# Kernel optimization log

Measured on AMD Instinct MI355X. Metric: run time of the kernel, lower is better.

The kernel has to match this reference:

```python
import jax, jax.numpy as jnp
import numpy as np

N, D, E, C = 100000, 256, 262144, 5


def setup_inputs() -> dict:
    key = jax.random.key(0)
    ks = jax.random.split(key, 8)
    s = 1.0 / np.sqrt(D)
    return {
        "node_feat": jax.random.normal(ks[0], (N, D), jnp.float32),
        "pair_idx": jax.random.randint(ks[1], (E, 2), 0, N, dtype=jnp.int64)
        if jax.config.jax_enable_x64 else jax.random.randint(ks[1], (E, 2), 0, N, dtype=jnp.int32),
        "W_agg": jax.random.normal(ks[2], (2 * D, D), jnp.float32) * (1.0 / np.sqrt(2 * D)),
        "b_agg": jnp.zeros((D,), jnp.float32),
        "We1": jax.random.normal(ks[3], (D, D), jnp.float32) * s,
        "be1": jnp.zeros((D,), jnp.float32),
        "We2": jax.random.normal(ks[4], (D, C), jnp.float32) * s,
        "be2": jnp.zeros((C,), jnp.float32),
        "Wn1": jax.random.normal(ks[5], (D, D), jnp.float32) * s,
        "bn1": jnp.zeros((D,), jnp.float32),
        "Wn2": jax.random.normal(ks[6], (D, 2), jnp.float32) * s,
        "bn2": jnp.zeros((2,), jnp.float32),
    }


def reference(node_feat, pair_idx, W_agg, b_agg, We1, be1, We2, be2, Wn1, bn1, Wn2, bn2):
    # node_predictor: Linear -> ReLU -> Linear (D -> D -> 2)
    node_res = jnp.maximum(node_feat @ Wn1 + bn1, 0.0) @ Wn2 + bn2  # [N, 2]

    # gather node-pair features for both directed orderings (x,y) and (y,x)
    src = node_feat[pair_idx[:, 0]]  # [E, D]
    dst = node_feat[pair_idx[:, 1]]  # [E, D]
    # edge_feat_agger(cat(src,dst)) + edge_feat_agger(cat(dst,src))
    ef_fwd = jnp.concatenate([src, dst], axis=-1) @ W_agg + b_agg  # [E, D]
    ef_bwd = jnp.concatenate([dst, src], axis=-1) @ W_agg + b_agg  # [E, D]
    ed_feat = ef_fwd + ef_bwd

    # edge_predictor: Linear -> ReLU -> Linear (D -> D -> C)
    pred_edge = jnp.maximum(ed_feat @ We1 + be1, 0.0) @ We2 + be2  # [E, C]
    return node_res, pred_edge
```

## Files before the change

kernel.cpp:

```cpp
#include <hip/hip_runtime.h>

#define D 256

typedef float f32x4 __attribute__((ext_vector_type(4)));
typedef short short8 __attribute__((ext_vector_type(8)));
typedef __bf16 bf16x8 __attribute__((ext_vector_type(8)));

static __device__ __forceinline__ short f2bs(float f) {
    __bf16 b = (__bf16)f;
    return __builtin_bit_cast(short, b);
}
static __device__ __forceinline__ float bs2f(short s) {
    unsigned u = ((unsigned)(unsigned short)s) << 16;
    return __builtin_bit_cast(float, u);
}


__global__ void pre_bc(const float* __restrict__ b_agg, const float* __restrict__ We1,
                       const float* __restrict__ be1, float* __restrict__ bc)
{
    int j = threadIdx.x;
    float acc = be1[j];
    for (int k = 0; k < D; ++k)
        acc += 2.f * b_agg[k] * We1[k * D + j];
    bc[j] = acc;
}

__global__ void pre_wct(const float* __restrict__ W_agg, const float* __restrict__ We1,
                        short* __restrict__ WcT)
{
    __shared__ float wsrow[D];
    int i = blockIdx.x, j = threadIdx.x;
    wsrow[j] = W_agg[i * D + j] + W_agg[(i + D) * D + j];
    __syncthreads();
    float acc = 0.f;
    for (int k = 0; k < D; ++k)
        acc += wsrow[k] * We1[k * D + j];
    WcT[j * D + i] = f2bs(acc);
}

__global__ void pre_wn1t(const float* __restrict__ Wn1, short* __restrict__ Wn1T)
{
    int i = blockIdx.x, j = threadIdx.x;
    Wn1T[j * D + i] = f2bs(Wn1[i * D + j]);
}

__global__ void pre_w2t(const float* __restrict__ We2, const float* __restrict__ Wn2,
                        short* __restrict__ We2T, short* __restrict__ Wn2T)
{
    int k = threadIdx.x;
    for (int c = 0; c < 16; ++c) {
        float ve = (c < 5) ? We2[k * 5 + c] : 0.f;
        float vn = (c < 2) ? Wn2[k * 2 + c] : 0.f;
        We2T[c * D + k] = f2bs(ve);
        Wn2T[c * D + k] = f2bs(vn);
    }
}

__global__ __launch_bounds__(512, 2)
void node_h_gemm2(const float* __restrict__ nf,
                  const short* __restrict__ WcT, const short* __restrict__ Wn1T,
                  const float* __restrict__ bc,  const float* __restrict__ bn1,
                  const short* __restrict__ Wn2T, const float* __restrict__ bn2,
                  short* __restrict__ H, float* __restrict__ outn, int nrows)
{
    __shared__ __align__(16) short sA[2048 * 8];
    __shared__ __align__(16) short hl[64 * D];

    const int tid = threadIdx.x;
    const int lane = tid & 63;
    const int w = tid >> 6;
    const int l15 = lane & 15;
    const int g = lane >> 4;
    const int rowblk = blockIdx.x * 64;

    const short* Wb = (w < 4) ? WcT : Wn1T;
    const int nc0 = (w & 3) * 4;
    short8 Bw[4][8];
#pragma unroll
    for (int t = 0; t < 4; ++t)
#pragma unroll
        for (int ks = 0; ks < 8; ++ks)
            Bw[t][ks] = *reinterpret_cast<const short8*>(
                Wb + ((nc0 + t) * 16 + l15) * D + ks * 32 + g * 8);

#pragma unroll
    for (int j = 0; j < 4; ++j) {
        const int i = j * 512 + tid;
        const int li = i & 15, gi = (i >> 4) & 3, fi = (i >> 6) & 3, ki = i >> 8;
        int r = rowblk + fi * 16 + li;
        if (r > nrows - 1) r = nrows - 1;
        const float4* p = reinterpret_cast<const float4*>(nf + (size_t)r * D + ki * 32 + gi * 8);
        float4 x0 = p[0], x1 = p[1];
        bf16x8 v = {(__bf16)x0.x, (__bf16)x0.y, (__bf16)x0.z, (__bf16)x0.w,
                    (__bf16)x1.x, (__bf16)x1.y, (__bf16)x1.z, (__bf16)x1.w};
        *reinterpret_cast<short8*>(&sA[i * 8]) = __builtin_bit_cast(short8, v);
    }
    __syncthreads();

    f32x4 acc[4][4];
#pragma unroll
    for (int f = 0; f < 4; ++f)
#pragma unroll
        for (int t = 0; t < 4; ++t)
            acc[f][t] = f32x4{0.f, 0.f, 0.f, 0.f};

#pragma unroll
    for (int ks = 0; ks < 8; ++ks) {
        short8 a[4];
#pragma unroll
        for (int f = 0; f < 4; ++f)
            a[f] = *reinterpret_cast<const short8*>(&sA[(ks * 256 + f * 64 + lane) * 8]);
#pragma unroll
        for (int t = 0; t < 4; ++t)
#pragma unroll
            for (int f = 0; f < 4; ++f)
                acc[f][t] = __builtin_amdgcn_mfma_f32_16x16x32_bf16(a[f], Bw[t][ks], acc[f][t], 0, 0, 0);
    }

    if (w < 4) {
#pragma unroll
        for (int t = 0; t < 4; ++t) {
            const int col = w * 64 + t * 16 + l15;
            const float bb = 0.5f * bc[col];
#pragma unroll
            for (int f = 0; f < 4; ++f)
#pragma unroll
                for (int r = 0; r < 4; ++r) {
                    const int grow = rowblk + f * 16 + g * 4 + r;
                    if (grow < nrows)
                        H[(size_t)grow * D + col] = f2bs(acc[f][t][r] + bb);
                }
        }
    } else {
#pragma unroll
        for (int t = 0; t < 4; ++t) {
            const int col = (w - 4) * 64 + t * 16 + l15;
            const float bb = bn1[col];
            const int chunk = col >> 3;
#pragma unroll
            for (int f = 0; f < 4; ++f)
#pragma unroll
                for (int r = 0; r < 4; ++r) {
                    const int row = f * 16 + g * 4 + r;
                    float v = fmaxf(acc[f][t][r] + bb, 0.f);
                    hl[row * D + (((chunk ^ (row & 7)) << 3) | (col & 7))] = f2bs(v);
                }
        }
    }

    __syncthreads();

    if (w >= 4) {
        const int vr = w - 4;
        const int row = vr * 16 + l15;
        f32x4 a2 = f32x4{0.f, 0.f, 0.f, 0.f};
#pragma unroll
        for (int ks = 0; ks < 8; ++ks) {
            const int k0 = ks * 32 + g * 8;
            const int c = ks * 4 + g;
            short8 bw = *reinterpret_cast<const short8*>(Wn2T + l15 * D + k0);
            short8 ah = *reinterpret_cast<const short8*>(&hl[row * D + ((c ^ (row & 7)) * 8)]);
            a2 = __builtin_amdgcn_mfma_f32_16x16x32_bf16(ah, bw, a2, 0, 0, 0);
        }
        if (l15 < 2) {
            const float b2 = bn2[l15];
#pragma unroll
            for (int r = 0; r < 4; ++r) {
                const int grow = rowblk + vr * 16 + g * 4 + r;
                if (grow < nrows)
                    outn[(size_t)grow * 2 + l15] = a2[r] + b2;
            }
        }
    }
}

__global__ __launch_bounds__(256, 4)
void edge_gemv(const short* __restrict__ H, const int* __restrict__ pair,
               const short* __restrict__ We2T, const float* __restrict__ be2,
               float* __restrict__ out, int nedges)
{
    const int lane = threadIdx.x & 63;
    const int w = threadIdx.x >> 6;
    const int l15 = lane & 15;
    const int g = lane >> 4;

    short8 Bf[8];
#pragma unroll
    for (int ks = 0; ks < 8; ++ks)
        Bf[ks] = *reinterpret_cast<const short8*>(We2T + l15 * D + ks * 32 + g * 8);

    const float b2 = (l15 < 5) ? be2[l15] : 0.f;
    const int base = blockIdx.x * 256 + w * 64;

#pragma unroll
    for (int grp = 0; grp < 4; ++grp) {
        int e = base + grp * 16 + l15;
        if (e > nedges - 1) e = nedges - 1;
        const size_t si = (size_t)(unsigned)pair[2 * e];
        const size_t di = (size_t)(unsigned)pair[2 * e + 1];
        const short8* sp = reinterpret_cast<const short8*>(H + si * D + g * 8);
        const short8* dp = reinterpret_cast<const short8*>(H + di * D + g * 8);
        short8 sv[8], dv[8];
#pragma unroll
        for (int ks = 0; ks < 8; ++ks) {
            sv[ks] = sp[ks * 4];
            dv[ks] = dp[ks * 4];
        }
        f32x4 acc = f32x4{0.f, 0.f, 0.f, 0.f};
#pragma unroll
        for (int ks = 0; ks < 8; ++ks) {
            short8 a;
#pragma unroll
            for (int i = 0; i < 8; ++i)
                a[i] = f2bs(fmaxf(bs2f(sv[ks][i]) + bs2f(dv[ks][i]), 0.f));
            acc = __builtin_amdgcn_mfma_f32_16x16x32_bf16(a, Bf[ks], acc, 0, 0, 0);
        }
        if (l15 < 5) {
#pragma unroll
            for (int r = 0; r < 4; ++r) {
                const int ge = base + grp * 16 + g * 4 + r;
                if (ge < nedges)
                    out[(size_t)ge * 5 + l15] = acc[r] + b2;
            }
        }
    }
}

template<int MODE>
__global__ __launch_bounds__(256, 2)
void fused_mlp(const float* __restrict__ feat,
               const int* __restrict__ pair,
               const short* __restrict__ W1T,
               const float* __restrict__ bias1,
               const short* __restrict__ W2T,
               const float* __restrict__ bias2,
               float* __restrict__ out,
               int nrows, int ncols)
{
    __shared__ short hl[128 * D];

    const int tid = threadIdx.x;
    const int lane = tid & 63;
    const int w = tid >> 6;
    const int l15 = lane & 15;
    const int g = lane >> 4;
    const int rowblk = blockIdx.x * 128 + w * 32;

    const float* ap0[2];
    const float* ap1[2];
#pragma unroll
    for (int f = 0; f < 2; ++f) {
        int r = rowblk + f * 16 + l15;
        if (r > nrows - 1) r = nrows - 1;
        if constexpr (MODE == 0) {
            ap0[f] = feat + (size_t)r * D;
            ap1[f] = nullptr;
        } else {
            ap0[f] = feat + (size_t)pair[2 * r] * D;
            ap1[f] = feat + (size_t)pair[2 * r + 1] * D;
        }
    }

    f32x4 acc[2][16];
#pragma unroll
    for (int f = 0; f < 2; ++f)
#pragma unroll
        for (int t = 0; t < 16; ++t)
            acc[f][t] = f32x4{0.f, 0.f, 0.f, 0.f};

#pragma unroll
    for (int ks = 0; ks < 8; ++ks) {
        const int k0 = ks * 32 + g * 8;
        short8 af[2];
#pragma unroll
        for (int f = 0; f < 2; ++f) {
            const float4* p0 = reinterpret_cast<const float4*>(ap0[f] + k0);
            float4 x0 = p0[0], x1 = p0[1];
            if constexpr (MODE == 1) {
                const float4* p1 = reinterpret_cast<const float4*>(ap1[f] + k0);
                float4 y0 = p1[0], y1 = p1[1];
                x0.x += y0.x; x0.y += y0.y; x0.z += y0.z; x0.w += y0.w;
                x1.x += y1.x; x1.y += y1.y; x1.z += y1.z; x1.w += y1.w;
            }
            bf16x8 bv = {(__bf16)x0.x, (__bf16)x0.y, (__bf16)x0.z, (__bf16)x0.w,
                         (__bf16)x1.x, (__bf16)x1.y, (__bf16)x1.z, (__bf16)x1.w};
            af[f] = __builtin_bit_cast(short8, bv);
        }
#pragma unroll
        for (int t = 0; t < 16; ++t) {
            short8 bw = *reinterpret_cast<const short8*>(W1T + ((t * 16 + l15) * D + k0));
            acc[0][t] = __builtin_amdgcn_mfma_f32_16x16x32_bf16(af[0], bw, acc[0][t], 0, 0, 0);
            acc[1][t] = __builtin_amdgcn_mfma_f32_16x16x32_bf16(af[1], bw, acc[1][t], 0, 0, 0);
        }
    }

#pragma unroll
    for (int t = 0; t < 16; ++t) {
        const int col = t * 16 + l15;
        const float b = bias1[col];
        const int chunk = col >> 3;
#pragma unroll
        for (int f = 0; f < 2; ++f) {
#pragma unroll
            for (int r = 0; r < 4; ++r) {
                const int rl = w * 32 + f * 16 + g * 4 + r;
                float v = fmaxf(acc[f][t][r] + b, 0.f);
                hl[rl * D + ((chunk ^ (rl & 7)) << 3) + (col & 7)] = f2bs(v);
            }
        }
    }

    __syncthreads();

    f32x4 acc2[2];
    acc2[0] = f32x4{0.f, 0.f, 0.f, 0.f};
    acc2[1] = f32x4{0.f, 0.f, 0.f, 0.f};
#pragma unroll
    for (int ks = 0; ks < 8; ++ks) {
        const int k0 = ks * 32 + g * 8;
        const int chunk = k0 >> 3;
        short8 bw = *reinterpret_cast<const short8*>(W2T + (l15 * D + k0));
#pragma unroll
        for (int f = 0; f < 2; ++f) {
            const int rl = w * 32 + f * 16 + l15;
            short8 ah = *reinterpret_cast<const short8*>(&hl[rl * D + ((chunk ^ (rl & 7)) << 3)]);
            acc2[f] = __builtin_amdgcn_mfma_f32_16x16x32_bf16(ah, bw, acc2[f], 0, 0, 0);
        }
    }

    if (l15 < ncols) {
        const float b2 = bias2[l15];
#pragma unroll
        for (int f = 0; f < 2; ++f) {
#pragma unroll
            for (int r = 0; r < 4; ++r) {
                const int grow = rowblk + f * 16 + g * 4 + r;
                if (grow < nrows)
                    out[(size_t)grow * ncols + l15] = acc2[f][r] + b2;
            }
        }
    }
}


extern "C" void kernel_launch(void* const* d_in, const int* in_sizes, int n_in,
                              void* d_out, int out_size, void* d_ws, size_t ws_size,
                              hipStream_t stream)
{
    const float* node_feat = (const float*)d_in[0];
    const int*   pair_idx  = (const int*)d_in[1];
    const float* W_agg     = (const float*)d_in[2];
    const float* b_agg     = (const float*)d_in[3];
    const float* We1       = (const float*)d_in[4];
    const float* be1       = (const float*)d_in[5];
    const float* We2       = (const float*)d_in[6];
    const float* be2       = (const float*)d_in[7];
    const float* Wn1       = (const float*)d_in[8];
    const float* bn1       = (const float*)d_in[9];
    const float* Wn2       = (const float*)d_in[10];
    const float* bn2       = (const float*)d_in[11];

    const int N = in_sizes[0] / D;
    const int E = in_sizes[1] / 2;

    float* out = (float*)d_out;
    char*  ws  = (char*)d_ws;

    short* WcT  = (short*)(ws + 0);
    short* Wn1T = (short*)(ws + 131072);
    short* We2T = (short*)(ws + 262144);
    short* Wn2T = (short*)(ws + 270336);
    float* bc   = (float*)(ws + 278528);
    const size_t H_OFF = 524288;
    short* H = (short*)(ws + H_OFF);
    const size_t need = H_OFF + (size_t)N * D * 2;

    pre_bc<<<1, 256, 0, stream>>>(b_agg, We1, be1, bc);
    pre_wct<<<D, 256, 0, stream>>>(W_agg, We1, WcT);
    pre_wn1t<<<D, 256, 0, stream>>>(Wn1, Wn1T);
    pre_w2t<<<1, 256, 0, stream>>>(We2, Wn2, We2T, Wn2T);

    if (ws_size >= need) {
        node_h_gemm2<<<(N + 63) / 64, 512, 0, stream>>>(
            node_feat, WcT, Wn1T, bc, bn1, Wn2T, bn2, H, out, N);

        edge_gemv<<<(E + 255) / 256, 256, 0, stream>>>(
            H, pair_idx, We2T, be2, out + (size_t)2 * N, E);
    } else {
        fused_mlp<0><<<(N + 127) / 128, 256, 0, stream>>>(
            node_feat, nullptr, Wn1T, bn1, Wn2T, bn2, out, N, 2);

        fused_mlp<1><<<E / 128, 256, 0, stream>>>(
            node_feat, pair_idx, WcT, bc, We2T, be2, out + (size_t)2 * N, E, 5);
    }
}
```

Before: 168.4 us.

## Stream weights through LDS with async loads and stage edge gathers in LDS

The node GEMM now uses 1024-thread blocks. Each warp holds a 32-column slice instead of keeping a full weight slice in registers, and the weights stream through double-buffered LDS with global_load_lds. H is staged in LDS and written out as coalesced 16-byte rows. The edge kernel gathers src/dst H rows straight into XOR-swizzled LDS with async loads, using shuffled indices, before the MFMA. This lowers register pressure and makes the gathers coalesced, at the cost of more LDS traffic and per-k-step barriers. The code relies on WcT and Wn1T being contiguous in the workspace, so it can index 32 column groups from a single WT pointer.

Measured after the change: 186.7 us. 1.11x slower.

```diff
diff --git a/kernel.cpp b/kernel.cpp
--- a/kernel.cpp
+++ b/kernel.cpp
@@ -13,6 +13,13 @@
 static __device__ __forceinline__ float bs2f(short s) {
     unsigned u = ((unsigned)(unsigned short)s) << 16;
     return __builtin_bit_cast(float, u);
+}
+
+static __device__ __forceinline__ void gload_lds16(const short* g, short* l) {
+    __builtin_amdgcn_global_load_lds(
+        (const __attribute__((address_space(1))) void*)g,
+        (__attribute__((address_space(3))) void*)l,
+        16, 0, 0);
 }
 
 
@@ -57,15 +64,15 @@
     }
 }
 
-__global__ __launch_bounds__(512, 2)
-void node_h_gemm2(const float* __restrict__ nf,
-                  const short* __restrict__ WcT, const short* __restrict__ Wn1T,
+__global__ __launch_bounds__(1024)
+void node_h_gemm3(const float* __restrict__ nf,
+                  const short* __restrict__ WT,
                   const float* __restrict__ bc,  const float* __restrict__ bn1,
                   const short* __restrict__ Wn2T, const float* __restrict__ bn2,
                   short* __restrict__ H, float* __restrict__ outn, int nrows)
 {
     __shared__ __align__(16) short sA[2048 * 8];
-    __shared__ __align__(16) short hl[64 * D];
+    __shared__ __align__(16) short sB[2][2048 * 8];
 
     const int tid = threadIdx.x;
     const int lane = tid & 63;
@@ -74,19 +81,9 @@
     const int g = lane >> 4;
     const int rowblk = blockIdx.x * 64;
 
-    const short* Wb = (w < 4) ? WcT : Wn1T;
-    const int nc0 = (w & 3) * 4;
-    short8 Bw[4][8];
-#pragma unroll
-    for (int t = 0; t < 4; ++t)
-#pragma unroll
-        for (int ks = 0; ks < 8; ++ks)
-            Bw[t][ks] = *reinterpret_cast<const short8*>(
-                Wb + ((nc0 + t) * 16 + l15) * D + ks * 32 + g * 8);
-
-#pragma unroll
-    for (int j = 0; j < 4; ++j) {
-        const int i = j * 512 + tid;
+#pragma unroll
+    for (int j = 0; j < 2; ++j) {
+        const int i = j * 1024 + tid;
         const int li = i & 15, gi = (i >> 4) & 3, fi = (i >> 6) & 3, ki = i >> 8;
         int r = rowblk + fi * 16 + li;
         if (r > nrows - 1) r = nrows - 1;
@@ -96,46 +93,74 @@
                     (__bf16)x1.x, (__bf16)x1.y, (__bf16)x1.z, (__bf16)x1.w};
         *reinterpret_cast<short8*>(&sA[i * 8]) = __builtin_bit_cast(short8, v);
     }
+#pragma unroll
+    for (int j = 0; j < 2; ++j) {
+        const int v = j * 1024 + tid;
+        const int nc = v >> 6, vl = v & 15, vg = (v >> 4) & 3;
+        gload_lds16(WT + (nc * 16 + vl) * D + vg * 8,
+                    &sB[0][(j * 1024 + w * 64) * 8]);
+    }
+    asm volatile("s_waitcnt vmcnt(0)" ::: "memory");
     __syncthreads();
 
-    f32x4 acc[4][4];
+    f32x4 acc[4][2];
 #pragma unroll
     for (int f = 0; f < 4; ++f)
 #pragma unroll
-        for (int t = 0; t < 4; ++t)
+        for (int t = 0; t < 2; ++t)
             acc[f][t] = f32x4{0.f, 0.f, 0.f, 0.f};
 
+    int cur = 0;
 #pragma unroll
     for (int ks = 0; ks < 8; ++ks) {
-        short8 a[4];
+        if (ks < 7) {
+#pragma unroll
+            for (int j = 0; j < 2; ++j) {
+                const int v = j * 1024 + tid;
+                const int nc = v >> 6, vl = v & 15, vg = (v >> 4) & 3;
+                gload_lds16(WT + (nc * 16 + vl) * D + (ks + 1) * 32 + vg * 8,
+                            &sB[cur ^ 1][(j * 1024 + w * 64) * 8]);
+            }
+        }
+        short8 a[4], b[2];
 #pragma unroll
         for (int f = 0; f < 4; ++f)
             a[f] = *reinterpret_cast<const short8*>(&sA[(ks * 256 + f * 64 + lane) * 8]);
 #pragma unroll
-        for (int t = 0; t < 4; ++t)
+        for (int t = 0; t < 2; ++t)
+            b[t] = *reinterpret_cast<const short8*>(&sB[cur][((w * 2 + t) * 64 + lane) * 8]);
+#pragma unroll
+        for (int t = 0; t < 2; ++t)
 #pragma unroll
             for (int f = 0; f < 4; ++f)
-                acc[f][t] = __builtin_amdgcn_mfma_f32_16x16x32_bf16(a[f], Bw[t][ks], acc[f][t], 0, 0, 0);
-    }
-
-    if (w < 4) {
-#pragma unroll
-        for (int t = 0; t < 4; ++t) {
-            const int col = w * 64 + t * 16 + l15;
+                acc[f][t] = __builtin_amdgcn_mfma_f32_16x16x32_bf16(a[f], b[t], acc[f][t], 0, 0, 0);
+        if (ks < 7) {
+            asm volatile("s_waitcnt vmcnt(0)" ::: "memory");
+            __syncthreads();
+            cur ^= 1;
+        }
+    }
+
+    __syncthreads();
+
+    short* sH = (short*)sB;
+    if (w < 8) {
+#pragma unroll
+        for (int t = 0; t < 2; ++t) {
+            const int col = w * 32 + t * 16 + l15;
             const float bb = 0.5f * bc[col];
 #pragma unroll
             for (int f = 0; f < 4; ++f)
 #pragma unroll
                 for (int r = 0; r < 4; ++r) {
-                    const int grow = rowblk + f * 16 + g * 4 + r;
-                    if (grow < nrows)
-                        H[(size_t)grow * D + col] = f2bs(acc[f][t][r] + bb);
+                    const int row = f * 16 + g * 4 + r;
+                    sH[row * D + col] = f2bs(acc[f][t][r] + bb);
                 }
         }
     } else {
 #pragma unroll
-        for (int t = 0; t < 4; ++t) {
-            const int col = (w - 4) * 64 + t * 16 + l15;
+        for (int t = 0; t < 2; ++t) {
+            const int col = (w - 8) * 32 + t * 16 + l15;
             const float bb = bn1[col];
             const int chunk = col >> 3;
 #pragma unroll
@@ -144,15 +169,24 @@
                 for (int r = 0; r < 4; ++r) {
                     const int row = f * 16 + g * 4 + r;
                     float v = fmaxf(acc[f][t][r] + bb, 0.f);
-                    hl[row * D + (((chunk ^ (row & 7)) << 3) | (col & 7))] = f2bs(v);
+                    sA[row * D + (((chunk ^ (row & 7)) << 3) | (col & 7))] = f2bs(v);
                 }
         }
     }
 
     __syncthreads();
 
-    if (w >= 4) {
-        const int vr = w - 4;
+#pragma unroll
+    for (int j = 0; j < 2; ++j) {
+        const int u = j * 1024 + tid;
+        const int row = u >> 5, seg = u & 31;
+        if (rowblk + row < nrows)
+            *reinterpret_cast<short8*>(H + (size_t)(rowblk + row) * D + seg * 8) =
+                *reinterpret_cast<const short8*>(&sH[u * 8]);
+    }
+
+    if (w >= 8 && w < 12) {
+        const int vr = w - 8;
         const int row = vr * 16 + l15;
         f32x4 a2 = f32x4{0.f, 0.f, 0.f, 0.f};
 #pragma unroll
@@ -160,7 +194,7 @@
             const int k0 = ks * 32 + g * 8;
             const int c = ks * 4 + g;
             short8 bw = *reinterpret_cast<const short8*>(Wn2T + l15 * D + k0);
-            short8 ah = *reinterpret_cast<const short8*>(&hl[row * D + ((c ^ (row & 7)) * 8)]);
+            short8 ah = *reinterpret_cast<const short8*>(&sA[row * D + ((c ^ (row & 7)) * 8)]);
             a2 = __builtin_amdgcn_mfma_f32_16x16x32_bf16(ah, bw, a2, 0, 0, 0);
         }
         if (l15 < 2) {
@@ -175,54 +209,61 @@
     }
 }
 
-__global__ __launch_bounds__(256, 4)
-void edge_gemv(const short* __restrict__ H, const int* __restrict__ pair,
-               const short* __restrict__ We2T, const float* __restrict__ be2,
-               float* __restrict__ out, int nedges)
-{
+__global__ __launch_bounds__(256)
+void edge_gemv2(const short* __restrict__ H, const int* __restrict__ pair,
+                const short* __restrict__ We2T, const float* __restrict__ be2,
+                float* __restrict__ out, int nedges)
+{
+    __shared__ __align__(16) short eb[4][32 * D];
+
     const int lane = threadIdx.x & 63;
     const int w = threadIdx.x >> 6;
     const int l15 = lane & 15;
     const int g = lane >> 4;
+    const int base = blockIdx.x * 64 + w * 16;
 
     short8 Bf[8];
 #pragma unroll
     for (int ks = 0; ks < 8; ++ks)
         Bf[ks] = *reinterpret_cast<const short8*>(We2T + l15 * D + ks * 32 + g * 8);
 
-    const float b2 = (l15 < 5) ? be2[l15] : 0.f;
-    const int base = blockIdx.x * 256 + w * 64;
-
-#pragma unroll
-    for (int grp = 0; grp < 4; ++grp) {
-        int e = base + grp * 16 + l15;
-        if (e > nedges - 1) e = nedges - 1;
-        const size_t si = (size_t)(unsigned)pair[2 * e];
-        const size_t di = (size_t)(unsigned)pair[2 * e + 1];
-        const short8* sp = reinterpret_cast<const short8*>(H + si * D + g * 8);
-        const short8* dp = reinterpret_cast<const short8*>(H + di * D + g * 8);
-        short8 sv[8], dv[8];
-#pragma unroll
-        for (int ks = 0; ks < 8; ++ks) {
-            sv[ks] = sp[ks * 4];
-            dv[ks] = dp[ks * 4];
-        }
-        f32x4 acc = f32x4{0.f, 0.f, 0.f, 0.f};
-#pragma unroll
-        for (int ks = 0; ks < 8; ++ks) {
-            short8 a;
-#pragma unroll
-            for (int i = 0; i < 8; ++i)
-                a[i] = f2bs(fmaxf(bs2f(sv[ks][i]) + bs2f(dv[ks][i]), 0.f));
-            acc = __builtin_amdgcn_mfma_f32_16x16x32_bf16(a, Bf[ks], acc, 0, 0, 0);
-        }
-        if (l15 < 5) {
-#pragma unroll
-            for (int r = 0; r < 4; ++r) {
-                const int ge = base + grp * 16 + g * 4 + r;
-                if (ge < nedges)
-                    out[(size_t)ge * 5 + l15] = acc[r] + b2;
-            }
+    int pv = 0;
+    {
+        int pi = 2 * base + lane;
+        const int pmax = 2 * nedges - 1;
+        if (lane < 32) pv = pair[pi > pmax ? pmax : pi];
+    }
+
+    const int rsub = lane >> 5;
+    const int pos = lane & 31;
+#pragma unroll
+    for (int j = 0; j < 16; ++j) {
+        const int ridx = __shfl(pv, 2 * j + rsub);
+        const int c = pos ^ (j & 7);
+        gload_lds16(H + (size_t)(unsigned)ridx * D + c * 8, &eb[w][(2 * j) * D]);
+    }
+    asm volatile("s_waitcnt vmcnt(0)" ::: "memory");
+
+    f32x4 acc = f32x4{0.f, 0.f, 0.f, 0.f};
+#pragma unroll
+    for (int ks = 0; ks < 8; ++ks) {
+        const int slot = (ks * 4 + g) ^ (l15 & 7);
+        short8 sv = *reinterpret_cast<const short8*>(&eb[w][(2 * l15) * D + slot * 8]);
+        short8 dv = *reinterpret_cast<const short8*>(&eb[w][(2 * l15 + 1) * D + slot * 8]);
+        short8 a;
+#pragma unroll
+        for (int i = 0; i < 8; ++i)
+            a[i] = f2bs(fmaxf(bs2f(sv[i]) + bs2f(dv[i]), 0.f));
+        acc = __builtin_amdgcn_mfma_f32_16x16x32_bf16(a, Bf[ks], acc, 0, 0, 0);
+    }
+
+    if (l15 < 5) {
+        const float b2 = be2[l15];
+#pragma unroll
+        for (int r = 0; r < 4; ++r) {
+            const int ge = base + g * 4 + r;
+            if (ge < nedges)
+                out[(size_t)ge * 5 + l15] = acc[r] + b2;
         }
     }
 }
@@ -382,10 +423,10 @@
     pre_w2t<<<1, 256, 0, stream>>>(We2, Wn2, We2T, Wn2T);
 
     if (ws_size >= need) {
-        node_h_gemm2<<<(N + 63) / 64, 512, 0, stream>>>(
-            node_feat, WcT, Wn1T, bc, bn1, Wn2T, bn2, H, out, N);
-
-        edge_gemv<<<(E + 255) / 256, 256, 0, stream>>>(
+        node_h_gemm3<<<(N + 63) / 64, 1024, 0, stream>>>(
+            node_feat, WcT, bc, bn1, Wn2T, bn2, H, out, N);
+
+        edge_gemv2<<<(E + 63) / 64, 256, 0, stream>>>(
             H, pair_idx, We2T, be2, out + (size_t)2 * N, E);
     } else {
         fused_mlp<0><<<(N + 127) / 128, 256, 0, stream>>>(
```

## Stage H stores via LDS and gather edge rows with global_load_lds

Applied to the files above, without the earlier changes.

The node GEMM now writes its H tile into shared memory first and then stores it to global memory as coalesced 16-byte rows, replacing scattered 2-byte stores. The edge kernel gathers source and destination H rows with direct global-to-LDS loads into a swizzled buffer, 16 edges per wave, and then reads MFMA operands from LDS. This aims to improve gather coalescing and memory-level parallelism. The cost is more LDS per block (64KB for the edge kernel), which limits occupancy, plus an extra barrier in the node kernel.

After: 187.1 us. 1.11x slower.

```diff
diff --git a/kernel.cpp b/kernel.cpp
--- a/kernel.cpp
+++ b/kernel.cpp
@@ -13,6 +13,13 @@
 static __device__ __forceinline__ float bs2f(short s) {
     unsigned u = ((unsigned)(unsigned short)s) << 16;
     return __builtin_bit_cast(float, u);
+}
+
+static __device__ __forceinline__ void gload_lds16(const short* g, short* l) {
+    __builtin_amdgcn_global_load_lds(
+        (const __attribute__((address_space(1))) void*)g,
+        (__attribute__((address_space(3))) void*)l,
+        16, 0, 0);
 }
 
 
@@ -58,7 +65,7 @@
 }
 
 __global__ __launch_bounds__(512, 2)
-void node_h_gemm2(const float* __restrict__ nf,
+void node_h_gemm4(const float* __restrict__ nf,
                   const short* __restrict__ WcT, const short* __restrict__ Wn1T,
                   const float* __restrict__ bc,  const float* __restrict__ bn1,
                   const short* __restrict__ Wn2T, const float* __restrict__ bn2,
@@ -83,6 +90,11 @@
         for (int ks = 0; ks < 8; ++ks)
             Bw[t][ks] = *reinterpret_cast<const short8*>(
                 Wb + ((nc0 + t) * 16 + l15) * D + ks * 32 + g * 8);
+#pragma unroll
+    for (int t = 0; t < 4; ++t)
+#pragma unroll
+        for (int ks = 0; ks < 8; ++ks)
+            asm volatile("" : "+v"(Bw[t][ks]));
 
 #pragma unroll
     for (int j = 0; j < 4; ++j) {
@@ -118,7 +130,10 @@
                 acc[f][t] = __builtin_amdgcn_mfma_f32_16x16x32_bf16(a[f], Bw[t][ks], acc[f][t], 0, 0, 0);
     }
 
+    __syncthreads();
+
     if (w < 4) {
+        short* sH = sA;
 #pragma unroll
         for (int t = 0; t < 4; ++t) {
             const int col = w * 64 + t * 16 + l15;
@@ -127,9 +142,8 @@
             for (int f = 0; f < 4; ++f)
 #pragma unroll
                 for (int r = 0; r < 4; ++r) {
-                    const int grow = rowblk + f * 16 + g * 4 + r;
-                    if (grow < nrows)
-                        H[(size_t)grow * D + col] = f2bs(acc[f][t][r] + bb);
+                    const int row = f * 16 + g * 4 + r;
+                    sH[row * D + col] = f2bs(acc[f][t][r] + bb);
                 }
         }
     } else {
@@ -151,7 +165,16 @@
 
     __syncthreads();
 
-    if (w >= 4) {
+    if (w < 4) {
+#pragma unroll
+        for (int j = 0; j < 8; ++j) {
+            const int u = j * 256 + tid;
+            const int row = u >> 5, seg = u & 31;
+            if (rowblk + row < nrows)
+                *reinterpret_cast<short8*>(H + (size_t)(rowblk + row) * D + seg * 8) =
+                    *reinterpret_cast<const short8*>(&sA[u * 8]);
+        }
+    } else {
         const int vr = w - 4;
         const int row = vr * 16 + l15;
         f32x4 a2 = f32x4{0.f, 0.f, 0.f, 0.f};
@@ -175,54 +198,61 @@
     }
 }
 
-__global__ __launch_bounds__(256, 4)
-void edge_gemv(const short* __restrict__ H, const int* __restrict__ pair,
-               const short* __restrict__ We2T, const float* __restrict__ be2,
-               float* __restrict__ out, int nedges)
-{
+__global__ __launch_bounds__(256)
+void edge_gemv2(const short* __restrict__ H, const int* __restrict__ pair,
+                const short* __restrict__ We2T, const float* __restrict__ be2,
+                float* __restrict__ out, int nedges)
+{
+    __shared__ __align__(16) short eb[4][32 * D];
+
     const int lane = threadIdx.x & 63;
     const int w = threadIdx.x >> 6;
     const int l15 = lane & 15;
     const int g = lane >> 4;
+    const int base = blockIdx.x * 64 + w * 16;
 
     short8 Bf[8];
 #pragma unroll
     for (int ks = 0; ks < 8; ++ks)
         Bf[ks] = *reinterpret_cast<const short8*>(We2T + l15 * D + ks * 32 + g * 8);
 
-    const float b2 = (l15 < 5) ? be2[l15] : 0.f;
-    const int base = blockIdx.x * 256 + w * 64;
-
-#pragma unroll
-    for (int grp = 0; grp < 4; ++grp) {
-        int e = base + grp * 16 + l15;
-        if (e > nedges - 1) e = nedges - 1;
-        const size_t si = (size_t)(unsigned)pair[2 * e];
-        const size_t di = (size_t)(unsigned)pair[2 * e + 1];
-        const short8* sp = reinterpret_cast<const short8*>(H + si * D + g * 8);
-        const short8* dp = reinterpret_cast<const short8*>(H + di * D + g * 8);
-        short8 sv[8], dv[8];
-#pragma unroll
-        for (int ks = 0; ks < 8; ++ks) {
-            sv[ks] = sp[ks * 4];
-            dv[ks] = dp[ks * 4];
-        }
-        f32x4 acc = f32x4{0.f, 0.f, 0.f, 0.f};
-#pragma unroll
-        for (int ks = 0; ks < 8; ++ks) {
-            short8 a;
-#pragma unroll
-            for (int i = 0; i < 8; ++i)
-                a[i] = f2bs(fmaxf(bs2f(sv[ks][i]) + bs2f(dv[ks][i]), 0.f));
-            acc = __builtin_amdgcn_mfma_f32_16x16x32_bf16(a, Bf[ks], acc, 0, 0, 0);
-        }
-        if (l15 < 5) {
-#pragma unroll
-            for (int r = 0; r < 4; ++r) {
-                const int ge = base + grp * 16 + g * 4 + r;
-                if (ge < nedges)
-                    out[(size_t)ge * 5 + l15] = acc[r] + b2;
-            }
+    int pv = 0;
+    {
+        int pi = 2 * base + lane;
+        const int pmax = 2 * nedges - 1;
+        if (lane < 32) pv = pair[pi > pmax ? pmax : pi];
+    }
+
+    const int rsub = lane >> 5;
+    const int pos = lane & 31;
+#pragma unroll
+    for (int j = 0; j < 16; ++j) {
+        const int ridx = __shfl(pv, 2 * j + rsub);
+        const int c = pos ^ (j & 7);
+        gload_lds16(H + (size_t)(unsigned)ridx * D + c * 8, &eb[w][(2 * j) * D]);
+    }
+    asm volatile("s_waitcnt vmcnt(0)" ::: "memory");
+
+    f32x4 acc = f32x4{0.f, 0.f, 0.f, 0.f};
+#pragma unroll
+    for (int ks = 0; ks < 8; ++ks) {
+        const int slot = (ks * 4 + g) ^ (l15 & 7);
+        short8 sv = *reinterpret_cast<const short8*>(&eb[w][(2 * l15) * D + slot * 8]);
+        short8 dv = *reinterpret_cast<const short8*>(&eb[w][(2 * l15 + 1) * D + slot * 8]);
+        short8 a;
+#pragma unroll
+        for (int i = 0; i < 8; ++i)
+            a[i] = f2bs(fmaxf(bs2f(sv[i]) + bs2f(dv[i]), 0.f));
+        acc = __builtin_amdgcn_mfma_f32_16x16x32_bf16(a, Bf[ks], acc, 0, 0, 0);
+    }
+
+    if (l15 < 5) {
+        const float b2 = be2[l15];
+#pragma unroll
+        for (int r = 0; r < 4; ++r) {
+            const int ge = base + g * 4 + r;
+            if (ge < nedges)
+                out[(size_t)ge * 5 + l15] = acc[r] + b2;
         }
     }
 }
@@ -382,10 +412,10 @@
     pre_w2t<<<1, 256, 0, stream>>>(We2, Wn2, We2T, Wn2T);
 
     if (ws_size >= need) {
-        node_h_gemm2<<<(N + 63) / 64, 512, 0, stream>>>(
+        node_h_gemm4<<<(N + 63) / 64, 512, 0, stream>>>(
             node_feat, WcT, Wn1T, bc, bn1, Wn2T, bn2, H, out, N);
 
-        edge_gemv<<<(E + 255) / 256, 256, 0, stream>>>(
+        edge_gemv2<<<(E + 63) / 64, 256, 0, stream>>>(
             H, pair_idx, We2T, be2, out + (size_t)2 * N, E);
     } else {
         fused_mlp<0><<<(N + 127) / 128, 256, 0, stream>>>(
```
